# Kernel tuning notes

Measured on AMD Instinct MI355X. Metric: run time of the kernel, lower is better.

## Reference

```python
import jax, jax.numpy as jnp
import numpy as np

TEMPERATURE = 0.5
EPS = 1e-8  # F.cosine_similarity eps


def _neg_mask_indices(B):
    # mask: ones, zero diagonal, zero the two positive off-diagonals
    N = 2 * B
    mask = np.ones((N, N), dtype=bool)
    np.fill_diagonal(mask, False)
    idx = np.arange(B)
    mask[idx, idx + B] = False
    mask[idx + B, idx] = False
    rows, cols = np.nonzero(mask)  # static, computed at trace time
    return rows, cols


def setup_inputs() -> dict:
    key = jax.random.key(0)
    k1, k2 = jax.random.split(key)
    B, D = 4096, 128
    z_i = jax.random.normal(k1, (B, D), dtype=jnp.float32)
    z_j = jax.random.normal(k2, (B, D), dtype=jnp.float32)
    return {"z_i": z_i, "z_j": z_j}


def reference(z_i, z_j):
    B = z_i.shape[0]
    N = 2 * B
    z = jnp.concatenate([z_i, z_j], axis=0)  # [N, D]
    norm = jnp.maximum(jnp.linalg.norm(z, axis=1, keepdims=True), EPS)
    zn = z / norm
    sim = (zn @ zn.T) / TEMPERATURE  # [N, N] cosine similarity / temp

    # positives: the i <-> i+B pairs
    sim_i_j = jnp.diagonal(sim, offset=B)
    sim_j_i = jnp.diagonal(sim, offset=-B)
    positives = jnp.concatenate([sim_i_j, sim_j_i], axis=0)[:, None]  # [N, 1]

    rows, cols = _neg_mask_indices(B)
    negatives = sim[rows, cols].reshape(N, N - 2)  # [N, N-2]

    logits = jnp.concatenate([positives, negatives], axis=1)  # [N, N-1]
    # cross-entropy with labels == 0 (positive is column 0)
    loss = jnp.mean(jax.nn.logsumexp(logits, axis=1) - logits[:, 0])
    return loss
```

## Files before the change

### kernel.cpp

```cpp
#include <hip/hip_runtime.h>
#include <hip/hip_bf16.h>
#include <math.h>


typedef __attribute__((ext_vector_type(8))) short bf16x8;
typedef __attribute__((ext_vector_type(4))) float f32x4;

#define NROWS 8192
#define DDIM  128
#define BHALF 4096
#define CHUNK 32
#define NT    32
#define NBLK  528
#define CPAD  264
#define SQRT_E2S 1.6986435980707531f
#define TWO_LN2  1.3862943611198906f
#define EXPDIAG  7.38905609893065f

static __device__ __forceinline__ unsigned short f2bf(float f) {
  unsigned int u = __float_as_uint(f);
  unsigned int r = (u + 0x7fffu + ((u >> 16) & 1u)) >> 16;
  return (unsigned short)r;
}

static __device__ __forceinline__ void glds16(const unsigned short* g, unsigned short* l) {
  __builtin_amdgcn_global_load_lds((const __attribute__((address_space(1))) unsigned int*)g,
                                   (__attribute__((address_space(3))) unsigned int*)l,
                                   16, 0, 0);
}

__global__ void norm_kernel(const float* __restrict__ zi, const float* __restrict__ zj,
                            unsigned short* __restrict__ zn,
                            float* __restrict__ row_sums, float* __restrict__ pos,
                            float* __restrict__ out) {
  __shared__ float2 xbuf[2][64];
  int wave = threadIdx.x >> 6;
  int lane = threadIdx.x & 63;
  int pi   = blockIdx.x * 2 + (wave & 1);
  int row  = pi + (wave >> 1) * BHALF;
  const float* src = (row < BHALF) ? (zi + (size_t)row * DDIM)
                                   : (zj + (size_t)(row - BHALF) * DDIM);
  float2 v = *(const float2*)(src + 2 * lane);
  float ss = v.x * v.x + v.y * v.y;
  #pragma unroll
  for (int off = 1; off < 64; off <<= 1) ss += __shfl_xor(ss, off);
  float scale = SQRT_E2S / fmaxf(sqrtf(ss), 1e-8f);
  v.x *= scale; v.y *= scale;
  unsigned int lo = f2bf(v.x), hi = f2bf(v.y);
  ((unsigned int*)(zn + (size_t)row * DDIM))[lane] = lo | (hi << 16);

  if (wave >= 2) xbuf[wave - 2][lane] = v;
  __syncthreads();
  if (wave < 2) {
    float2 w = xbuf[wave][lane];
    float d = v.x * w.x + v.y * w.y;
    #pragma unroll
    for (int off = 1; off < 64; off <<= 1) d += __shfl_xor(d, off);
    if (lane == 0) pos[pi] = d;
  }
  if (threadIdx.x < 4) row_sums[blockIdx.x * 4 + threadIdx.x] = 0.0f;
  if (blockIdx.x == 0 && threadIdx.x == 4) out[0] = 0.0f;
}

__global__ __launch_bounds__(256, 2)
void sim_kernel(const unsigned short* __restrict__ zn, float* __restrict__ row_sums) {
  __shared__ unsigned short lds[2 * CHUNK * DDIM];
  __shared__ float colpart[16][CPAD];

  int t = blockIdx.x;
  int tx = (int)((65.0f - sqrtf((float)(4225 - 8 * t))) * 0.5f);
  while ((tx + 1) * NT - ((tx + 1) * tx) / 2 <= t) ++tx;
  while (tx * NT - (tx * (tx - 1)) / 2 > t) --tx;
  const int ty = t - (tx * NT - (tx * (tx - 1)) / 2) + tx;
  const bool diag = (tx == ty);

  const int wave = threadIdx.x >> 6;
  const int lane = threadIdx.x & 63;
  const int l15  = lane & 15;
  const int quad = lane >> 4;

  const int row_base = tx * 256 + wave * 64;
  const int col_base = ty * 256;

  bf16x8 a[4][4];
  const unsigned short* abase = zn + (size_t)(row_base + l15) * DDIM + quad * 8;
  #pragma unroll
  for (int mi = 0; mi < 4; ++mi)
    #pragma unroll
    for (int kf = 0; kf < 4; ++kf)
      a[mi][kf] = *(const bf16x8*)(abase + mi * 16 * DDIM + kf * 32);

  float rs[4][4];
  #pragma unroll
  for (int mi = 0; mi < 4; ++mi)
    #pragma unroll
    for (int r = 0; r < 4; ++r) rs[mi][r] = 0.0f;

  const int t0 = wave * 64 + lane;
  const int r0 = t0 >> 4,         c0 = (t0 & 15) ^ (r0 & 15);
  const int r1 = (t0 + 256) >> 4, c1 = (t0 & 15) ^ (r1 & 15);
  const unsigned short* gst0 = zn + (size_t)(col_base + r0) * DDIM + c0 * 8;
  const unsigned short* gst1 = zn + (size_t)(col_base + r1) * DDIM + c1 * 8;

  int rdoff[4];
  #pragma unroll
  for (int kf = 0; kf < 4; ++kf)
    rdoff[kf] = l15 * DDIM + (((quad + 4 * kf) ^ l15) << 3);

  float* cp = &colpart[wave * 4 + quad][l15];

  glds16(gst0, lds + wave * 512);
  glds16(gst1, lds + 2048 + wave * 512);
  __syncthreads();

  for (int ch = 0; ch < 8; ++ch) {
    const int buf = ch & 1;
    if (ch < 7) {
      const unsigned short* g0 = gst0 + (size_t)(ch + 1) * CHUNK * DDIM;
      const unsigned short* g1 = gst1 + (size_t)(ch + 1) * CHUNK * DDIM;
      unsigned short* lb = lds + ((ch + 1) & 1) * 4096;
      glds16(g0, lb + wave * 512);
      glds16(g1, lb + 2048 + wave * 512);
    }
    const unsigned short* lb = lds + buf * 4096;
    #pragma unroll
    for (int ni = 0; ni < 2; ++ni) {
      bf16x8 b[4];
      #pragma unroll
      for (int kf = 0; kf < 4; ++kf)
        b[kf] = *(const bf16x8*)(lb + ni * 16 * DDIM + rdoff[kf]);
      f32x4 acc[4];
      #pragma unroll
      for (int mi = 0; mi < 4; ++mi) {
        f32x4 z = {0.0f, 0.0f, 0.0f, 0.0f};
        acc[mi] = __builtin_amdgcn_mfma_f32_16x16x32_bf16(a[mi][0], b[0], z, 0, 0, 0);
      }
      #pragma unroll
      for (int kf = 1; kf < 4; ++kf)
        #pragma unroll
        for (int mi = 0; mi < 4; ++mi)
          acc[mi] = __builtin_amdgcn_mfma_f32_16x16x32_bf16(a[mi][kf], b[kf], acc[mi], 0, 0, 0);
      float cs = 0.0f;
      #pragma unroll
      for (int mi = 0; mi < 4; ++mi)
        #pragma unroll
        for (int r = 0; r < 4; ++r) {
          float e = __builtin_amdgcn_exp2f(acc[mi][r]);
          rs[mi][r] += e;
          cs += e;
        }
      cp[(ch * 2 + ni) * 16] = cs;
    }
    __syncthreads();
  }

  #pragma unroll
  for (int mi = 0; mi < 4; ++mi)
    #pragma unroll
    for (int r = 0; r < 4; ++r) {
      float v = rs[mi][r];
      v += __shfl_xor(v, 1);
      v += __shfl_xor(v, 2);
      v += __shfl_xor(v, 4);
      v += __shfl_xor(v, 8);
      if (l15 == 0)
        atomicAdd(&row_sums[row_base + mi * 16 + quad * 4 + r], v);
    }
  if (!diag) {
    float v = 0.0f;
    #pragma unroll
    for (int s = 0; s < 16; ++s) v += colpart[s][threadIdx.x];
    atomicAdd(&row_sums[col_base + threadIdx.x], v);
  }
}

__global__ void finalize_kernel(const float* __restrict__ row_sums,
                                const float* __restrict__ pos,
                                float* __restrict__ out) {
  __shared__ float red[4];
  int i = blockIdx.x * 256 + threadIdx.x;
  float si = row_sums[i] - EXPDIAG;
  float sp = row_sums[i + BHALF] - EXPDIAG;
  float v = logf(si) + logf(sp) - TWO_LN2 * pos[i];
  #pragma unroll
  for (int off = 1; off < 64; off <<= 1) v += __shfl_xor(v, off);
  int wave = threadIdx.x >> 6, lane = threadIdx.x & 63;
  if (lane == 0) red[wave] = v;
  __syncthreads();
  if (threadIdx.x == 0)
    atomicAdd(out, (red[0] + red[1] + red[2] + red[3]) * (1.0f / 8192.0f));
}

extern "C" void kernel_launch(void* const* d_in, const int* in_sizes, int n_in,
                              void* d_out, int out_size, void* d_ws, size_t ws_size,
                              hipStream_t stream) {
  const float* zi = (const float*)d_in[0];
  const float* zj = (const float*)d_in[1];
  char* ws = (char*)d_ws;
  unsigned short* zn = (unsigned short*)ws;
  float* row_sums = (float*)(ws + (size_t)NROWS * DDIM * 2);
  float* pos      = (float*)(ws + (size_t)NROWS * DDIM * 2 + NROWS * 4);
  float* out = (float*)d_out;

  norm_kernel<<<2048, 256, 0, stream>>>(zi, zj, zn, row_sums, pos, out);
  sim_kernel<<<NBLK, 256, 0, stream>>>(zn, row_sums);
  finalize_kernel<<<16, 256, 0, stream>>>(row_sums, pos, out);
}
```

Baseline: 95.35 us.

## Shrink similarity tiles to 128 and replace row-sum atomics with per-tile partials

Tiles in the triangular similarity kernel shrink from 256 to 128, raising the block count from 528 to 2080 to improve load balance across CUs. Each wave now owns 32 rows instead of 64, so each block does less reuse of its A fragments. Row and column exp-sums are no longer accumulated with atomics into a zeroed buffer. Each tile writes its sums into a distinct slot of a [64, N] partial buffer, and the finalize kernel adds up the 64 slots per row. This removes atomic contention and the zeroing step, but finalize now reads a larger partial buffer with only 16 blocks.

Result: faster. 86.53 us (-9.3%).

```diff
diff --git a/kernel.cpp b/kernel.cpp
--- a/kernel.cpp
+++ b/kernel.cpp
@@ -10,9 +10,10 @@
 #define DDIM  128
 #define BHALF 4096
 #define CHUNK 32
-#define NT    32
-#define NBLK  528
-#define CPAD  264
+#define TILE  128
+#define NT    64
+#define NBLK  2080
+#define CPAD  136
 #define SQRT_E2S 1.6986435980707531f
 #define TWO_LN2  1.3862943611198906f
 #define EXPDIAG  7.38905609893065f
@@ -31,8 +32,7 @@
 
 __global__ void norm_kernel(const float* __restrict__ zi, const float* __restrict__ zj,
                             unsigned short* __restrict__ zn,
-                            float* __restrict__ row_sums, float* __restrict__ pos,
-                            float* __restrict__ out) {
+                            float* __restrict__ pos, float* __restrict__ out) {
   __shared__ float2 xbuf[2][64];
   int wave = threadIdx.x >> 6;
   int lane = threadIdx.x & 63;
@@ -58,17 +58,16 @@
     for (int off = 1; off < 64; off <<= 1) d += __shfl_xor(d, off);
     if (lane == 0) pos[pi] = d;
   }
-  if (threadIdx.x < 4) row_sums[blockIdx.x * 4 + threadIdx.x] = 0.0f;
-  if (blockIdx.x == 0 && threadIdx.x == 4) out[0] = 0.0f;
+  if (blockIdx.x == 0 && threadIdx.x == 0) out[0] = 0.0f;
 }
 
 __global__ __launch_bounds__(256, 2)
-void sim_kernel(const unsigned short* __restrict__ zn, float* __restrict__ row_sums) {
+void sim_kernel(const unsigned short* __restrict__ zn, float* __restrict__ part) {
   __shared__ unsigned short lds[2 * CHUNK * DDIM];
   __shared__ float colpart[16][CPAD];
 
   int t = blockIdx.x;
-  int tx = (int)((65.0f - sqrtf((float)(4225 - 8 * t))) * 0.5f);
+  int tx = (int)((129.0f - sqrtf((float)(16641 - 8 * t))) * 0.5f);
   while ((tx + 1) * NT - ((tx + 1) * tx) / 2 <= t) ++tx;
   while (tx * NT - (tx * (tx - 1)) / 2 > t) --tx;
   const int ty = t - (tx * NT - (tx * (tx - 1)) / 2) + tx;
@@ -79,20 +78,20 @@
   const int l15  = lane & 15;
   const int quad = lane >> 4;
 
-  const int row_base = tx * 256 + wave * 64;
-  const int col_base = ty * 256;
-
-  bf16x8 a[4][4];
+  const int row_base = tx * TILE + wave * 32;
+  const int col_base = ty * TILE;
+
+  bf16x8 a[2][4];
   const unsigned short* abase = zn + (size_t)(row_base + l15) * DDIM + quad * 8;
   #pragma unroll
-  for (int mi = 0; mi < 4; ++mi)
+  for (int mi = 0; mi < 2; ++mi)
     #pragma unroll
     for (int kf = 0; kf < 4; ++kf)
       a[mi][kf] = *(const bf16x8*)(abase + mi * 16 * DDIM + kf * 32);
 
-  float rs[4][4];
-  #pragma unroll
-  for (int mi = 0; mi < 4; ++mi)
+  float rs[2][4];
+  #pragma unroll
+  for (int mi = 0; mi < 2; ++mi)
     #pragma unroll
     for (int r = 0; r < 4; ++r) rs[mi][r] = 0.0f;
 
@@ -113,9 +112,9 @@
   glds16(gst1, lds + 2048 + wave * 512);
   __syncthreads();
 
-  for (int ch = 0; ch < 8; ++ch) {
+  for (int ch = 0; ch < 4; ++ch) {
     const int buf = ch & 1;
-    if (ch < 7) {
+    if (ch < 3) {
       const unsigned short* g0 = gst0 + (size_t)(ch + 1) * CHUNK * DDIM;
       const unsigned short* g1 = gst1 + (size_t)(ch + 1) * CHUNK * DDIM;
       unsigned short* lb = lds + ((ch + 1) & 1) * 4096;
@@ -129,20 +128,20 @@
       #pragma unroll
       for (int kf = 0; kf < 4; ++kf)
         b[kf] = *(const bf16x8*)(lb + ni * 16 * DDIM + rdoff[kf]);
-      f32x4 acc[4];
-      #pragma unroll
-      for (int mi = 0; mi < 4; ++mi) {
+      f32x4 acc[2];
+      #pragma unroll
+      for (int mi = 0; mi < 2; ++mi) {
         f32x4 z = {0.0f, 0.0f, 0.0f, 0.0f};
         acc[mi] = __builtin_amdgcn_mfma_f32_16x16x32_bf16(a[mi][0], b[0], z, 0, 0, 0);
       }
       #pragma unroll
       for (int kf = 1; kf < 4; ++kf)
         #pragma unroll
-        for (int mi = 0; mi < 4; ++mi)
+        for (int mi = 0; mi < 2; ++mi)
           acc[mi] = __builtin_amdgcn_mfma_f32_16x16x32_bf16(a[mi][kf], b[kf], acc[mi], 0, 0, 0);
       float cs = 0.0f;
       #pragma unroll
-      for (int mi = 0; mi < 4; ++mi)
+      for (int mi = 0; mi < 2; ++mi)
         #pragma unroll
         for (int r = 0; r < 4; ++r) {
           float e = __builtin_amdgcn_exp2f(acc[mi][r]);
@@ -155,7 +154,7 @@
   }
 
   #pragma unroll
-  for (int mi = 0; mi < 4; ++mi)
+  for (int mi = 0; mi < 2; ++mi)
     #pragma unroll
     for (int r = 0; r < 4; ++r) {
       float v = rs[mi][r];
@@ -164,23 +163,29 @@
       v += __shfl_xor(v, 4);
       v += __shfl_xor(v, 8);
       if (l15 == 0)
-        atomicAdd(&row_sums[row_base + mi * 16 + quad * 4 + r], v);
+        part[(size_t)ty * NROWS + row_base + mi * 16 + quad * 4 + r] = v;
     }
-  if (!diag) {
+  if (!diag && threadIdx.x < TILE) {
     float v = 0.0f;
     #pragma unroll
     for (int s = 0; s < 16; ++s) v += colpart[s][threadIdx.x];
-    atomicAdd(&row_sums[col_base + threadIdx.x], v);
-  }
-}
-
-__global__ void finalize_kernel(const float* __restrict__ row_sums,
+    part[(size_t)tx * NROWS + col_base + threadIdx.x] = v;
+  }
+}
+
+__global__ void finalize_kernel(const float* __restrict__ part,
                                 const float* __restrict__ pos,
                                 float* __restrict__ out) {
   __shared__ float red[4];
   int i = blockIdx.x * 256 + threadIdx.x;
-  float si = row_sums[i] - EXPDIAG;
-  float sp = row_sums[i + BHALF] - EXPDIAG;
+  float si = 0.0f, sp = 0.0f;
+  #pragma unroll 8
+  for (int s = 0; s < NT; ++s) {
+    si += part[(size_t)s * NROWS + i];
+    sp += part[(size_t)s * NROWS + i + BHALF];
+  }
+  si -= EXPDIAG;
+  sp -= EXPDIAG;
   float v = logf(si) + logf(sp) - TWO_LN2 * pos[i];
   #pragma unroll
   for (int off = 1; off < 64; off <<= 1) v += __shfl_xor(v, off);
@@ -198,11 +203,12 @@
   const float* zj = (const float*)d_in[1];
   char* ws = (char*)d_ws;
   unsigned short* zn = (unsigned short*)ws;
-  float* row_sums = (float*)(ws + (size_t)NROWS * DDIM * 2);
-  float* pos      = (float*)(ws + (size_t)NROWS * DDIM * 2 + NROWS * 4);
+  float* part = (float*)(ws + (size_t)NROWS * DDIM * 2);
+  float* pos  = (float*)(ws + (size_t)NROWS * DDIM * 2
+                            + (size_t)NT * NROWS * 4);
   float* out = (float*)d_out;
 
-  norm_kernel<<<2048, 256, 0, stream>>>(zi, zj, zn, row_sums, pos, out);
-  sim_kernel<<<NBLK, 256, 0, stream>>>(zn, row_sums);
-  finalize_kernel<<<16, 256, 0, stream>>>(row_sums, pos, out);
-}
+  norm_kernel<<<2048, 256, 0, stream>>>(zi, zj, zn, pos, out);
+  sim_kernel<<<NBLK, 256, 0, stream>>>(zn, part);
+  finalize_kernel<<<16, 256, 0, stream>>>(part, pos, out);
+}
```
